# Performance work log

Hardware: AMD Instinct MI355X
Metric: run time of the kernel (lower is better)

Reference implementation:

```python
import jax, jax.numpy as jnp
import numpy as np

HEADS = 4
ATTN_DIM = 32
SCALE = ATTN_DIM ** -0.5
EPS = 1e-12  # F.normalize eps


def rmsnorm_chan(x, g):
    # x: (b, c, h, w); RMSNorm over channel dim: F.normalize(x, dim=1) * g * sqrt(c)
    c = x.shape[1]
    n = jnp.sqrt(jnp.sum(x * x, axis=1, keepdims=True))
    return x / jnp.maximum(n, EPS) * g[None, :, None, None] * jnp.sqrt(jnp.asarray(c, x.dtype))


def setup_inputs() -> dict:
    key = jax.random.key(0)
    ks = jax.random.split(key, 4)
    b, c, h, w = 16, 256, 64, 64
    hidden = HEADS * ATTN_DIM  # 128
    x = jax.random.normal(ks[0], (b, c, h, w), dtype=jnp.float32)
    norm_g = jnp.ones((c,), jnp.float32)
    w_qkv = jax.random.normal(ks[1], (3 * hidden, c), dtype=jnp.float32) * 0.02
    mem_kv = jax.random.normal(ks[2], (2, HEADS, ATTN_DIM, 4), dtype=jnp.float32)
    w_out = jax.random.normal(ks[3], (c, hidden), dtype=jnp.float32) * 0.02
    b_out = jnp.zeros((c,), jnp.float32)
    out_norm_g = jnp.ones((c,), jnp.float32)
    return {"x": x, "norm_g": norm_g, "w_qkv": w_qkv, "mem_kv": mem_kv,
            "w_out": w_out, "b_out": b_out, "out_norm_g": out_norm_g}


def reference(x, norm_g, w_qkv, mem_kv, w_out, b_out, out_norm_g):
    b, c, h, w = x.shape
    n = h * w
    xn = rmsnorm_chan(x, norm_g).reshape(b, c, n)  # pre-norm, flatten spatial
    # 1x1 conv (no bias) == channel matmul: (b, 3*hidden, n)
    qkv = jnp.einsum('oc,bcn->bon', w_qkv, xn)
    q, k, v = jnp.split(qkv, 3, axis=1)
    # (b, heads, d, n)
    q = q.reshape(b, HEADS, ATTN_DIM, n)
    k = k.reshape(b, HEADS, ATTN_DIM, n)
    v = v.reshape(b, HEADS, ATTN_DIM, n)
    # prepend memory kv (broadcast over batch): (b, heads, d, num_mem + n)
    mk = jnp.broadcast_to(mem_kv[0][None], (b, HEADS, ATTN_DIM, mem_kv.shape[-1]))
    mv = jnp.broadcast_to(mem_kv[1][None], (b, HEADS, ATTN_DIM, mem_kv.shape[-1]))
    k = jnp.concatenate([mk, k], axis=-1)
    v = jnp.concatenate([mv, v], axis=-1)
    q = jax.nn.softmax(q, axis=-2) * SCALE  # softmax over feature dim d
    k = jax.nn.softmax(k, axis=-1)          # softmax over token dim n
    context = jnp.einsum('bhdn,bhen->bhde', k, v)   # small d x e per head
    out = jnp.einsum('bhde,bhdn->bhen', context, q)  # (b, heads, e, n)
    out = out.reshape(b, HEADS * ATTN_DIM, h, w)
    # 1x1 conv with bias, then RMSNorm
    out = jnp.einsum('oc,bchw->bohw', w_out, out) + b_out[None, :, None, None]
    return rmsnorm_chan(out, out_norm_g)
```

## Files before the change

kernel.cpp:

```cpp
#include <hip/hip_runtime.h>
#include <hip/hip_bf16.h>

typedef __hip_bfloat16 bf16;
typedef __attribute__((ext_vector_type(8))) short bf16x8;
typedef __attribute__((ext_vector_type(4))) float floatx4;

#define NB 16
#define NC 256
#define NPIX 4096
#define NHID 128
#define NH 4
#define ND 32
#define NMEM 4
#define QSCALE 0.17677669529663687f

#define LGKM0()  asm volatile("s_waitcnt lgkmcnt(0)" ::: "memory")

__launch_bounds__(256)
__global__ void kW(const float* __restrict__ wqkv, const float* __restrict__ g,
                   bf16* __restrict__ wgpack, float* __restrict__ zbase){
  const int u = blockIdx.x*256 + threadIdx.x;
  for (int z = u; z < 65536 + 2048; z += 48*256) zbase[z] = 0.f;
  const int s = u / 1536;
  const int r = u - s*1536;
  const int tile = r >> 6, l = r & 63;
  const int row = tile*16 + (l & 15);
  const int kb  = s*32 + (l >> 4)*8;
  const float* wp = wqkv + (size_t)row*NC + kb;
  floatx4 w0 = *(const floatx4*)wp;
  floatx4 w1 = *(const floatx4*)(wp + 4);
  floatx4 g0 = *(const floatx4*)(g + kb);
  floatx4 g1 = *(const floatx4*)(g + kb + 4);
  alignas(16) bf16 tmp[8];
  #pragma unroll
  for (int i = 0; i < 4; ++i){
    tmp[i]   = __float2bfloat16(w0[i]*g0[i]);
    tmp[4+i] = __float2bfloat16(w1[i]*g1[i]);
  }
  *(uint4*)(wgpack + (size_t)u*8) = *(const uint4*)tmp;
}

__launch_bounds__(256)
__global__ void kA(const float* __restrict__ x, const bf16* __restrict__ wgpack,
                   float* __restrict__ dout,
                   float* __restrict__ ctxu, float* __restrict__ zacc){
  __shared__ char smem alignas(16) [38144];
  bf16 (*Pb)[72] = (bf16(*)[72])smem;
  bf16 (*Vb)[72] = (bf16(*)[72])(smem + 18432);
  float* ssqL = (float*)(smem + 36864);
  float* sL   = (float*)(smem + 37888);
  const int t = threadIdx.x;
  const int pb = blockIdx.x * 64, b = blockIdx.y;
  const int wv = t >> 6, lane = t & 63, m = lane & 15, q4 = lane >> 4;
  const int px_st = t & 63, cg_st = t >> 6;
  const float* xb = x + (size_t)b*NC*NPIX;
  float ssq = 0.f;
  float xr[2][8];
  bf16x8 af[2][6];

  auto xissue = [&](int c, float* dst){
    const float* xp = xb + (size_t)(c*32 + cg_st*8)*NPIX + pb + px_st;
    #pragma unroll
    for (int j = 0; j < 8; ++j) dst[j] = xp[(size_t)j*NPIX];
  };
  auto xwrite = [&](int c, const float* v){
    alignas(16) bf16 tmp[8];
    #pragma unroll
    for (int j = 0; j < 8; ++j){
      ssq += v[j]*v[j];
      tmp[j] = __float2bfloat16(v[j]);
    }
    bf16 (*Xb)[40] = (bf16(*)[40])(smem + (c&1)*5120);
    *(uint4*)&Xb[px_st][cg_st*8] = *(const uint4*)tmp;
  };
  auto wload = [&](int c, int rt)->bf16x8 {
    return *(const bf16x8*)(wgpack + ((size_t)(c*24 + wv*6 + rt)*64 + lane)*8);
  };

  xissue(0, xr[0]);
  #pragma unroll
  for (int rt = 0; rt < 6; ++rt) af[0][rt] = wload(0, rt);
  xissue(1, xr[1]);
  xwrite(0, xr[0]);
  LGKM0();
  __builtin_amdgcn_s_barrier();

  floatx4 acc[6][4] = {};
  #pragma unroll 1
  for (int s2 = 0; s2 < 8; s2 += 2){
    {
      bf16 (*Xb)[40] = (bf16(*)[40])(smem + 0);
      bf16x8 bfr[4];
      #pragma unroll
      for (int pt = 0; pt < 4; ++pt)
        bfr[pt] = *(const bf16x8*)&Xb[pt*16 + m][q4*8];
      #pragma unroll
      for (int rt = 0; rt < 6; ++rt) af[1][rt] = wload(s2 + 1, rt);
      if (s2 < 6) xissue(s2 + 2, xr[0]);
      #pragma unroll
      for (int rt = 0; rt < 6; ++rt)
        #pragma unroll
        for (int pt = 0; pt < 4; ++pt)
          acc[rt][pt] = __builtin_amdgcn_mfma_f32_16x16x32_bf16(af[0][rt], bfr[pt], acc[rt][pt], 0, 0, 0);
      xwrite(s2 + 1, xr[1]);
      LGKM0();
      __builtin_amdgcn_s_barrier();
    }
    {
      bf16 (*Xb)[40] = (bf16(*)[40])(smem + 5120);
      bf16x8 bfr[4];
      #pragma unroll
      for (int pt = 0; pt < 4; ++pt)
        bfr[pt] = *(const bf16x8*)&Xb[pt*16 + m][q4*8];
      if (s2 < 6){
        #pragma unroll
        for (int rt = 0; rt < 6; ++rt) af[0][rt] = wload(s2 + 2, rt);
      }
      if (s2 < 6) xissue(s2 + 3, xr[1]);
      #pragma unroll
      for (int rt = 0; rt < 6; ++rt)
        #pragma unroll
        for (int pt = 0; pt < 4; ++pt)
          acc[rt][pt] = __builtin_amdgcn_mfma_f32_16x16x32_bf16(af[1][rt], bfr[pt], acc[rt][pt], 0, 0, 0);
      if (s2 < 6) xwrite(s2 + 2, xr[0]);
      LGKM0();
      __builtin_amdgcn_s_barrier();
    }
  }
  ssqL[cg_st*64 + px_st] = ssq;
  __syncthreads();
  if (t < 64){
    float tot = ssqL[t] + ssqL[64 + t] + ssqL[128 + t] + ssqL[192 + t];
    sL[t] = 16.0f / fmaxf(sqrtf(tot), 1e-12f);
  }
  __syncthreads();
  float sv[4];
  #pragma unroll
  for (int pt = 0; pt < 4; ++pt) sv[pt] = sL[pt*16 + m];
  #pragma unroll
  for (int pr = 0; pr < 3; ++pr){
    const int ra = 2*pr, rb = 2*pr + 1;
    const int row0 = wv*96 + pr*32;
    const int type = row0 >> 7;
    if (type == 0){
      const int slice = row0 >> 5;
      const int j0 = (q4 & 1)*4;
      #pragma unroll
      for (int pt = 0; pt < 4; ++pt){
        float va[4], vb[4];
        float mx = -1e30f;
        #pragma unroll
        for (int r = 0; r < 4; ++r){
          va[r] = acc[ra][pt][r]*sv[pt];
          vb[r] = acc[rb][pt][r]*sv[pt];
          mx = fmaxf(mx, fmaxf(va[r], vb[r]));
        }
        mx = fmaxf(mx, __shfl_xor(mx, 16, 64));
        mx = fmaxf(mx, __shfl_xor(mx, 32, 64));
        float se = 0.f;
        #pragma unroll
        for (int r = 0; r < 4; ++r){
          va[r] = __expf(va[r] - mx); vb[r] = __expf(vb[r] - mx);
          se += va[r] + vb[r];
        }
        se += __shfl_xor(se, 16, 64);
        se += __shfl_xor(se, 32, 64);
        const float inv = QSCALE / se;
        alignas(8) bf16 pka[4], pkb[4];
        #pragma unroll
        for (int r = 0; r < 4; ++r){
          pka[r] = __float2bfloat16(va[r]*inv);
          pkb[r] = __float2bfloat16(vb[r]*inv);
        }
        const int ca = (slice*4 + pt)*4 + (q4 >> 1);
        const int cb = ca + 2;
        bf16* pa = (bf16*)(dout + (size_t)(b*NC + ca)*NPIX + pb) + m*8 + j0;
        bf16* pv = (bf16*)(dout + (size_t)(b*NC + cb)*NPIX + pb) + m*8 + j0;
        *(uint2*)pa = *(const uint2*)pka;
        *(uint2*)pv = *(const uint2*)pkb;
      }
    } else if (type == 1){
      const int d0 = row0 - 128;
      float za[4] = {}, zb[4] = {};
      #pragma unroll
      for (int pt = 0; pt < 4; ++pt){
        #pragma unroll
        for (int r = 0; r < 4; ++r){
          float pa = __expf(acc[ra][pt][r]*sv[pt]);
          float pv = __expf(acc[rb][pt][r]*sv[pt]);
          za[r] += pa; zb[r] += pv;
          Pb[d0      + q4*4 + r][pt*16 + m] = __float2bfloat16(pa);
          Pb[d0 + 16 + q4*4 + r][pt*16 + m] = __float2bfloat16(pv);
        }
      }
      #pragma unroll
      for (int r = 0; r < 4; ++r){
        #pragma unroll
        for (int o = 1; o < 16; o <<= 1){
          za[r] += __shfl_xor(za[r], o, 64);
          zb[r] += __shfl_xor(zb[r], o, 64);
        }
      }
      if (m == 0){
        #pragma unroll
        for (int r = 0; r < 4; ++r){
          atomicAdd(&zacc[b*NHID + d0      + q4*4 + r], za[r]);
          atomicAdd(&zacc[b*NHID + d0 + 16 + q4*4 + r], zb[r]);
        }
      }
    } else {
      const int v0 = row0 - 256;
      #pragma unroll
      for (int pt = 0; pt < 4; ++pt)
        #pragma unroll
        for (int r = 0; r < 4; ++r){
          Vb[v0      + q4*4 + r][pt*16 + m] = __float2bfloat16(acc[ra][pt][r]*sv[pt]);
          Vb[v0 + 16 + q4*4 + r][pt*16 + m] = __float2bfloat16(acc[rb][pt][r]*sv[pt]);
        }
    }
  }
  __syncthreads();
  floatx4 cx[2][2] = {};
  #pragma unroll
  for (int k0t = 0; k0t < 64; k0t += 32){
    bf16x8 af2[2], bf2[2];
    #pragma unroll
    for (int dt = 0; dt < 2; ++dt) af2[dt] = *(const bf16x8*)&Pb[wv*32 + dt*16 + m][k0t + q4*8];
    #pragma unroll
    for (int et = 0; et < 2; ++et) bf2[et] = *(const bf16x8*)&Vb[wv*32 + et*16 + m][k0t + q4*8];
    #pragma unroll
    for (int dt = 0; dt < 2; ++dt)
      #pragma unroll
      for (int et = 0; et < 2; ++et)
        cx[dt][et] = __builtin_amdgcn_mfma_f32_16x16x32_bf16(af2[dt], bf2[et], cx[dt][et], 0, 0, 0);
  }
  float* cb2 = ctxu + (size_t)(b*NH + wv)*ND*ND;
  #pragma unroll
  for (int dt = 0; dt < 2; ++dt)
    #pragma unroll
    for (int et = 0; et < 2; ++et)
      #pragma unroll
      for (int r = 0; r < 4; ++r)
        atomicAdd(&cb2[(dt*16 + q4*4 + r)*ND + et*16 + m], cx[dt][et][r]);
}

__launch_bounds__(256)
__global__ void k4_weff(const float* __restrict__ ctxu, const float* __restrict__ zacc,
                        const float* __restrict__ memkv, const float* __restrict__ wout,
                        bf16* __restrict__ wpack){
  __shared__ float ctxL[4][32][32];
  __shared__ float woutL[64][129];
  const int t = threadIdx.x;
  const int o0 = blockIdx.x * 64, b = blockIdx.y;
  {
    const float* ws = wout + (size_t)o0*NHID;
    #pragma unroll
    for (int i = 0; i < 32; ++i){
      const int idx = i*256 + t;
      woutL[idx >> 7][idx & 127] = ws[idx];
    }
  }
  if (t < 128){
    const int h = t >> 5;
    const float* mk = memkv + t*NMEM;
    float me[4]; float z = zacc[b*NHID + t];
    #pragma unroll
    for (int j = 0; j < 4; ++j){ me[j] = __expf(mk[j]); z += me[j]; }
    const float invz = 1.0f / z;
    const float* cp = ctxu + (size_t)(b*NH*ND + t)*ND;
    const float* mv = memkv + (size_t)(NHID + h*ND)*NMEM;
    #pragma unroll
    for (int e = 0; e < ND; ++e){
      float ce = cp[e];
      #pragma unroll
      for (int j = 0; j < 4; ++j) ce += me[j]*mv[e*NMEM + j];
      ctxL[h][t & 31][e] = ce * invz;
    }
  }
  __syncthreads();
  const int ol = t & 63, g = t >> 6;
  float out[32] = {};
  #pragma unroll
  for (int e = 0; e < 32; ++e){
    const float we = woutL[ol][g*32 + e];
    #pragma unroll
    for (int d = 0; d < 32; ++d) out[d] += ctxL[g][d][e] * we;
  }
  const int o = o0 + ol, tile = o >> 4, m16 = o & 15;
  #pragma unroll
  for (int q4k = 0; q4k < 4; ++q4k){
    alignas(16) bf16 tmp[8];
    #pragma unroll
    for (int j = 0; j < 8; ++j) tmp[j] = __float2bfloat16(out[q4k*8 + j]);
    *(uint4*)(wpack + ((size_t)((b*4 + g)*16 + tile)*64 + q4k*16 + m16)*8) = *(const uint4*)tmp;
  }
}

__launch_bounds__(256)
__global__ void k5_out(float* dout, const bf16* __restrict__ wpack,
                       const float* __restrict__ bout, const float* __restrict__ gout){
  __shared__ float red[256];
  __shared__ float nf[64];
  const int t = threadIdx.x;
  const int pb = blockIdx.x * 64, b = blockIdx.y;
  const int wv = t >> 6, lane = t & 63, m = lane & 15, q4 = lane >> 4;
  bf16x8 wf[2][4], qf[2][4];
  auto loadw = [&](int s, bf16x8* dst){
    #pragma unroll
    for (int rt = 0; rt < 4; ++rt)
      dst[rt] = *(const bf16x8*)(wpack + ((size_t)((b*4 + s)*16 + wv*4 + rt)*64 + lane)*8);
  };
  auto loadq = [&](int s, bf16x8* dst){
    #pragma unroll
    for (int pt = 0; pt < 4; ++pt)
      dst[pt] = *(const bf16x8*)((const char*)(dout + (size_t)(b*NC + (s*4 + pt)*4 + q4)*NPIX + pb) + m*16);
  };
  loadw(0, wf[0]); loadq(0, qf[0]);
  loadw(1, wf[1]); loadq(1, qf[1]);
  floatx4 acc[4][4] = {};
  #pragma unroll
  for (int s = 0; s < 4; ++s){
    const int buf = s & 1;
    #pragma unroll
    for (int rt = 0; rt < 4; ++rt)
      #pragma unroll
      for (int pt = 0; pt < 4; ++pt)
        acc[rt][pt] = __builtin_amdgcn_mfma_f32_16x16x32_bf16(wf[buf][rt], qf[buf][pt], acc[rt][pt], 0, 0, 0);
    if (s < 2){ loadw(s + 2, wf[buf]); loadq(s + 2, qf[buf]); }
  }
  float ps[4] = {0.f, 0.f, 0.f, 0.f};
  #pragma unroll
  for (int rt = 0; rt < 4; ++rt){
    const int row = wv*64 + rt*16 + q4*4;
    #pragma unroll
    for (int r = 0; r < 4; ++r){
      const float bias = bout[row + r];
      #pragma unroll
      for (int pt = 0; pt < 4; ++pt){
        acc[rt][pt][r] += bias;
        ps[pt] += acc[rt][pt][r]*acc[rt][pt][r];
      }
    }
  }
  #pragma unroll
  for (int pt = 0; pt < 4; ++pt){
    ps[pt] += __shfl_xor(ps[pt], 16, 64);
    ps[pt] += __shfl_xor(ps[pt], 32, 64);
  }
  if (q4 == 0){
    #pragma unroll
    for (int pt = 0; pt < 4; ++pt) red[wv*64 + pt*16 + m] = ps[pt];
  }
  __syncthreads();
  if (t < 64){
    float tot = red[t] + red[64 + t] + red[128 + t] + red[192 + t];
    nf[t] = 16.0f / fmaxf(sqrtf(tot), 1e-12f);
  }
  __syncthreads();
  float nv[4];
  #pragma unroll
  for (int pt = 0; pt < 4; ++pt) nv[pt] = nf[pt*16 + m];
  #pragma unroll
  for (int rt = 0; rt < 4; ++rt){
    const int row = wv*64 + rt*16 + q4*4;
    #pragma unroll
    for (int r = 0; r < 4; ++r){
      const float gg = gout[row + r];
      float* op = dout + (size_t)(b*NC + row + r)*NPIX + pb + m;
      #pragma unroll
      for (int pt = 0; pt < 4; ++pt)
        op[pt*16] = acc[rt][pt][r]*nv[pt]*gg;
    }
  }
}

extern "C" void kernel_launch(void* const* d_in, const int* in_sizes, int n_in,
                              void* d_out, int out_size, void* d_ws, size_t ws_size,
                              hipStream_t stream) {
  (void)in_sizes; (void)n_in; (void)out_size; (void)ws_size;
  const float* x     = (const float*)d_in[0];
  const float* ng    = (const float*)d_in[1];
  const float* wqkv  = (const float*)d_in[2];
  const float* memkv = (const float*)d_in[3];
  const float* wout  = (const float*)d_in[4];
  const float* bout  = (const float*)d_in[5];
  const float* gout  = (const float*)d_in[6];
  float* dout = (float*)d_out;
  char* ws = (char*)d_ws;
  bf16*  wgpack = (bf16*)(ws);
  bf16*  wpack  = (bf16*)(ws + 196608);
  float* ctxu   = (float*)(ws + 1245184);
  float* zacc   = (float*)(ws + 1507328);

  kW     <<<dim3(48),      256, 0, stream>>>(wqkv, ng, wgpack, ctxu);
  kA     <<<dim3(64, 16),  256, 0, stream>>>(x, wgpack, dout, ctxu, zacc);
  k4_weff<<<dim3(4, 16),   256, 0, stream>>>(ctxu, zacc, memkv, wout, wpack);
  k5_out <<<dim3(64, 16),  256, 0, stream>>>(dout, wpack, bout, gout);
}
```

Baseline: 194.5 us.

## Split x transpose and bf16 conversion into separate kernel, load MFMA operands directly

Result: slower. 200.4 us (+3.0%).

```diff
diff --git a/kernel.cpp b/kernel.cpp
--- a/kernel.cpp
+++ b/kernel.cpp
@@ -13,8 +13,6 @@
 #define ND 32
 #define NMEM 4
 #define QSCALE 0.17677669529663687f
-
-#define LGKM0()  asm volatile("s_waitcnt lgkmcnt(0)" ::: "memory")
 
 __launch_bounds__(256)
 __global__ void kW(const float* __restrict__ wqkv, const float* __restrict__ g,
@@ -41,102 +39,90 @@
 }
 
 __launch_bounds__(256)
-__global__ void kA(const float* __restrict__ x, const bf16* __restrict__ wgpack,
-                   float* __restrict__ dout,
+__global__ void kT(const float* __restrict__ x, bf16* __restrict__ xt,
+                   float* __restrict__ sLg){
+  __shared__ bf16 XL[64][264];
+  __shared__ float ssqL[256];
+  const int t = threadIdx.x;
+  const int pb = blockIdx.x*64, b = blockIdx.y;
+  const int px = t & 63, cg = t >> 6;
+  const float* xb = x + (size_t)b*NC*NPIX + pb + px;
+  float ssq = 0.f;
+  #pragma unroll
+  for (int s4 = 0; s4 < 8; ++s4){
+    const float* xp = xb + (size_t)(s4*32 + cg*8)*NPIX;
+    alignas(16) bf16 tmp[8];
+    #pragma unroll
+    for (int j = 0; j < 8; ++j){
+      float v = xp[(size_t)j*NPIX];
+      ssq += v*v;
+      tmp[j] = __float2bfloat16(v);
+    }
+    *(uint4*)&XL[px][s4*32 + cg*8] = *(const uint4*)tmp;
+  }
+  ssqL[cg*64 + px] = ssq;
+  __syncthreads();
+  if (t < 64){
+    float tot = ssqL[t] + ssqL[64 + t] + ssqL[128 + t] + ssqL[192 + t];
+    sLg[(size_t)b*NPIX + pb + t] = 16.0f / fmaxf(sqrtf(tot), 1e-12f);
+  }
+  bf16* xr = xt + ((size_t)b*NPIX + pb)*NC;
+  const int p = t >> 2, c0 = t & 3;
+  #pragma unroll
+  for (int k = 0; k < 8; ++k){
+    const int c = c0 + k*4;
+    *(uint4*)(xr + (size_t)p*NC + c*8) = *(const uint4*)&XL[p][c*8];
+  }
+}
+
+__launch_bounds__(256)
+__global__ void kA(const bf16* __restrict__ xt, const bf16* __restrict__ wgpack,
+                   const float* __restrict__ sLg, float* __restrict__ dout,
                    float* __restrict__ ctxu, float* __restrict__ zacc){
-  __shared__ char smem alignas(16) [38144];
+  __shared__ char smem alignas(16) [36864];
   bf16 (*Pb)[72] = (bf16(*)[72])smem;
   bf16 (*Vb)[72] = (bf16(*)[72])(smem + 18432);
-  float* ssqL = (float*)(smem + 36864);
-  float* sL   = (float*)(smem + 37888);
   const int t = threadIdx.x;
   const int pb = blockIdx.x * 64, b = blockIdx.y;
   const int wv = t >> 6, lane = t & 63, m = lane & 15, q4 = lane >> 4;
-  const int px_st = t & 63, cg_st = t >> 6;
-  const float* xb = x + (size_t)b*NC*NPIX;
-  float ssq = 0.f;
-  float xr[2][8];
-  bf16x8 af[2][6];
-
-  auto xissue = [&](int c, float* dst){
-    const float* xp = xb + (size_t)(c*32 + cg_st*8)*NPIX + pb + px_st;
-    #pragma unroll
-    for (int j = 0; j < 8; ++j) dst[j] = xp[(size_t)j*NPIX];
-  };
-  auto xwrite = [&](int c, const float* v){
-    alignas(16) bf16 tmp[8];
-    #pragma unroll
-    for (int j = 0; j < 8; ++j){
-      ssq += v[j]*v[j];
-      tmp[j] = __float2bfloat16(v[j]);
-    }
-    bf16 (*Xb)[40] = (bf16(*)[40])(smem + (c&1)*5120);
-    *(uint4*)&Xb[px_st][cg_st*8] = *(const uint4*)tmp;
-  };
+  const bf16* xrow = xt + ((size_t)b*NPIX + pb)*NC;
+
   auto wload = [&](int c, int rt)->bf16x8 {
     return *(const bf16x8*)(wgpack + ((size_t)(c*24 + wv*6 + rt)*64 + lane)*8);
   };
-
-  xissue(0, xr[0]);
+  auto xload = [&](int s, int pt)->bf16x8 {
+    return *(const bf16x8*)(xrow + (size_t)(pt*16 + m)*NC + s*32 + q4*8);
+  };
+
+  bf16x8 af[2][6], bfr[2][4];
   #pragma unroll
   for (int rt = 0; rt < 6; ++rt) af[0][rt] = wload(0, rt);
-  xissue(1, xr[1]);
-  xwrite(0, xr[0]);
-  LGKM0();
-  __builtin_amdgcn_s_barrier();
+  #pragma unroll
+  for (int pt = 0; pt < 4; ++pt) bfr[0][pt] = xload(0, pt);
+  #pragma unroll
+  for (int rt = 0; rt < 6; ++rt) af[1][rt] = wload(1, rt);
+  #pragma unroll
+  for (int pt = 0; pt < 4; ++pt) bfr[1][pt] = xload(1, pt);
 
   floatx4 acc[6][4] = {};
-  #pragma unroll 1
-  for (int s2 = 0; s2 < 8; s2 += 2){
-    {
-      bf16 (*Xb)[40] = (bf16(*)[40])(smem + 0);
-      bf16x8 bfr[4];
+  #pragma unroll
+  for (int s = 0; s < 8; ++s){
+    const int cur = s & 1;
+    #pragma unroll
+    for (int rt = 0; rt < 6; ++rt)
       #pragma unroll
       for (int pt = 0; pt < 4; ++pt)
-        bfr[pt] = *(const bf16x8*)&Xb[pt*16 + m][q4*8];
-      #pragma unroll
-      for (int rt = 0; rt < 6; ++rt) af[1][rt] = wload(s2 + 1, rt);
-      if (s2 < 6) xissue(s2 + 2, xr[0]);
-      #pragma unroll
-      for (int rt = 0; rt < 6; ++rt)
-        #pragma unroll
-        for (int pt = 0; pt < 4; ++pt)
-          acc[rt][pt] = __builtin_amdgcn_mfma_f32_16x16x32_bf16(af[0][rt], bfr[pt], acc[rt][pt], 0, 0, 0);
-      xwrite(s2 + 1, xr[1]);
-      LGKM0();
-      __builtin_amdgcn_s_barrier();
-    }
-    {
-      bf16 (*Xb)[40] = (bf16(*)[40])(smem + 5120);
-      bf16x8 bfr[4];
-      #pragma unroll
-      for (int pt = 0; pt < 4; ++pt)
-        bfr[pt] = *(const bf16x8*)&Xb[pt*16 + m][q4*8];
-      if (s2 < 6){
-        #pragma unroll
-        for (int rt = 0; rt < 6; ++rt) af[0][rt] = wload(s2 + 2, rt);
-      }
-      if (s2 < 6) xissue(s2 + 3, xr[1]);
-      #pragma unroll
-      for (int rt = 0; rt < 6; ++rt)
-        #pragma unroll
-        for (int pt = 0; pt < 4; ++pt)
-          acc[rt][pt] = __builtin_amdgcn_mfma_f32_16x16x32_bf16(af[1][rt], bfr[pt], acc[rt][pt], 0, 0, 0);
-      if (s2 < 6) xwrite(s2 + 2, xr[0]);
-      LGKM0();
-      __builtin_amdgcn_s_barrier();
-    }
-  }
-  ssqL[cg_st*64 + px_st] = ssq;
-  __syncthreads();
-  if (t < 64){
-    float tot = ssqL[t] + ssqL[64 + t] + ssqL[128 + t] + ssqL[192 + t];
-    sL[t] = 16.0f / fmaxf(sqrtf(tot), 1e-12f);
-  }
-  __syncthreads();
+        acc[rt][pt] = __builtin_amdgcn_mfma_f32_16x16x32_bf16(af[cur][rt], bfr[cur][pt], acc[rt][pt], 0, 0, 0);
+    if (s < 6){
+      #pragma unroll
+      for (int rt = 0; rt < 6; ++rt) af[cur][rt] = wload(s + 2, rt);
+      #pragma unroll
+      for (int pt = 0; pt < 4; ++pt) bfr[cur][pt] = xload(s + 2, pt);
+    }
+  }
   float sv[4];
   #pragma unroll
-  for (int pt = 0; pt < 4; ++pt) sv[pt] = sL[pt*16 + m];
+  for (int pt = 0; pt < 4; ++pt) sv[pt] = sLg[(size_t)b*NPIX + pb + pt*16 + m];
   #pragma unroll
   for (int pr = 0; pr < 3; ++pr){
     const int ra = 2*pr, rb = 2*pr + 1;
@@ -391,9 +377,12 @@
   bf16*  wpack  = (bf16*)(ws + 196608);
   float* ctxu   = (float*)(ws + 1245184);
   float* zacc   = (float*)(ws + 1507328);
+  float* sLg    = (float*)(ws + 1515520);
+  bf16*  xt     = (bf16*)(ws + 1777664);
 
   kW     <<<dim3(48),      256, 0, stream>>>(wqkv, ng, wgpack, ctxu);
-  kA     <<<dim3(64, 16),  256, 0, stream>>>(x, wgpack, dout, ctxu, zacc);
+  kT     <<<dim3(64, 16),  256, 0, stream>>>(x, xt, sLg);
+  kA     <<<dim3(64, 16),  256, 0, stream>>>(xt, wgpack, sLg, dout, ctxu, zacc);
   k4_weff<<<dim3(4, 16),   256, 0, stream>>>(ctxu, zacc, memkv, wout, wpack);
   k5_out <<<dim3(64, 16),  256, 0, stream>>>(dout, wpack, bout, gout);
 }
```
